# Kernel tuning notes

Measured on AMD Instinct MI355X. Metric: run time of the kernel, lower is better.

## Reference

```python
import jax, jax.numpy as jnp
import numpy as np

B, IN_CH, OUT_CH, R = 16, 32, 32, 32
M1, M2 = 32, 32          # n_modes; must equal in_ch for the torch 2D branch to run
H, W = 256, 256


def setup_inputs() -> dict:
    key = jax.random.key(0)
    k1, k2, k3, k4 = jax.random.split(key, 4)
    x = jax.random.normal(k1, (B, IN_CH, H, W), jnp.float32)
    coeff_real = jax.random.normal(k2, (R, M1, M2, IN_CH), jnp.float32)
    coeff_imag = jax.random.normal(k3, (R, M1, M2, IN_CH), jnp.float32)
    proj = jax.random.normal(k4, (OUT_CH, R), jnp.float32)
    return {"x": x, "coeff_real": coeff_real, "coeff_imag": coeff_imag, "proj": proj}


def reference(x, coeff_real, coeff_imag, proj):
    # rfftn over the last 2 dims -> (B, C, H, W//2+1) complex64
    x_ft = jnp.fft.rfftn(x, axes=(-2, -1))
    coeff = (coeff_real + 1j * coeff_imag).astype(jnp.complex64)  # (R, M1, M2, IN)
    # W = einsum('or, r...i -> o...i') -> axes (OUT, M1, M2, IN)
    Wt = jnp.einsum('or,rabi->oabi', proj.astype(jnp.complex64), coeff)
    Hf, Wf = x_ft.shape[-2], x_ft.shape[-1]
    m1 = min(M1, Hf)   # torch loop bound over i
    m2 = min(M2, Wf)   # torch loop bound over j
    # Faithful to torch indexing: w_slice = W[..., i, j] has shape (OUT, M1) and is
    # contracted against the CHANNEL axis of x_ft. So effectively:
    #   out_ft[b,o,i,j] = sum_c x_ft[b,c,i,j] * Wt[o, c, i, j]
    # where Wt's axis1 (the 'm1' axis) is indexed by channel c.
    sub = jnp.einsum('bcij,ocij->boij', x_ft[..., :m1, :m2], Wt[:, :, :m1, :m2])
    out_ft = jnp.zeros((x.shape[0], OUT_CH, Hf, Wf), jnp.complex64)
    out_ft = out_ft.at[..., :m1, :m2].set(sub.astype(jnp.complex64))
    return jnp.fft.irfftn(out_ft, s=(x.shape[-2], x.shape[-1]), axes=(-2, -1))
```

## Files before the change

### kernel.cpp

```cpp
#include <hip/hip_runtime.h>
#include <math.h>


#define THETA (6.283185307179586f / 256.0f)

typedef float f32x4 __attribute__((ext_vector_type(4)));
typedef __bf16 bf16x8 __attribute__((ext_vector_type(8)));

__device__ __forceinline__ ushort f2bf(float f) {
    uint b = __float_as_uint(f);
    b += 0x7FFF + ((b >> 16) & 1);
    return (ushort)(b >> 16);
}
__device__ __forceinline__ ushort bfc(float f) {
    __bf16 h = (__bf16)f;
    return __builtin_bit_cast(ushort, h);
}

__global__ void kSetup(const float* __restrict__ proj, const float* __restrict__ cr,
                       const float* __restrict__ ci, ushort* __restrict__ Dbf,
                       ushort* __restrict__ Gbf, ushort* __restrict__ Ebf,
                       float2* __restrict__ Wt) {
    int blk = blockIdx.x, tid = threadIdx.x;
    if (blk < 64) {
        float s, c;
        int jr = blk, w = tid;
        __sincosf((((jr >> 1) * w) & 255) * THETA, &s, &c);
        Dbf[jr * 256 + w] = (jr & 1) ? f2bf(-s) : f2bf(c);
        Gbf[w * 64 + jr]  = (jr & 1) ? f2bf(s)  : f2bf(c);
        return;
    }
    if (blk < 128) {
        float s, c;
        int e = (blk - 64) * 256 + tid;
        int h = e >> 6, ir = e & 63;
        __sincosf((((ir >> 1) * h) & 255) * THETA, &s, &c);
        Ebf[h * 64 + ir] = (ir & 1) ? f2bf(-s) : f2bf(c);
        return;
    }
    __shared__ float2 co[32][33];
    __shared__ float pr[32 * 32];
    int bb = blk - 128;
    int c = bb >> 5;
    int i = bb & 31;
    for (int idx = tid; idx < 1024; idx += 256) pr[idx] = proj[idx];
    for (int idx = tid; idx < 1024; idx += 256) {
        int r = idx >> 5, j = idx & 31;
        int g = ((r * 32 + c) * 32 + i) * 32 + j;
        co[r][j] = make_float2(cr[g], ci[g]);
    }
    __syncthreads();
    int j = tid & 31, og = tid >> 5;
    for (int oo = 0; oo < 4; ++oo) {
        int o = og * 4 + oo;
        float wr = 0.f, wi = 0.f;
        #pragma unroll
        for (int r = 0; r < 32; ++r) {
            float p = pr[o * 32 + r];
            float2 v = co[r][j];
            wr += p * v.x;
            wi += p * v.y;
        }
        Wt[((o * 32 + c) * 32 + i) * 32 + j] = make_float2(wr, wi);
    }
}

__global__ void __launch_bounds__(512) kA(const float* __restrict__ x,
                                          const ushort* __restrict__ Dbf,
                                          float2* __restrict__ Xf) {
    __shared__ __align__(16) ushort Dl[64 * 264];
    __shared__ __align__(16) ushort Yl[64 * 264];
    int bc = blockIdx.x;
    int tid = threadIdx.x;
    int l = tid & 63, wv = tid >> 6;
    int lr = l & 15, kg = l >> 4;

    {
        const uint4* ds = (const uint4*)Dbf;
        #pragma unroll
        for (int q = 0; q < 4; ++q) {
            int idx = tid + 512 * q;
            int row = idx >> 5, c8 = idx & 31;
            *(uint4*)&Dl[row * 264 + c8 * 8] = ds[idx];
        }
    }
    __syncthreads();

    const float* xp = x + (size_t)bc * 65536;

    #pragma unroll
    for (int hh = 0; hh < 2; ++hh) {
        f32x4 acc1[4];
        #pragma unroll
        for (int mt = 0; mt < 4; ++mt) acc1[mt] = (f32x4){0.f, 0.f, 0.f, 0.f};
        const f32x4* rp = (const f32x4*)(xp + (size_t)(hh * 128 + wv * 16 + lr) * 256)
                          + kg * 2;
        #pragma unroll
        for (int wh = 0; wh < 2; ++wh) {
            f32x4 xv[8];
            #pragma unroll
            for (int ks = 0; ks < 4; ++ks) {
                xv[2 * ks]     = rp[wh * 32 + ks * 8];
                xv[2 * ks + 1] = rp[wh * 32 + ks * 8 + 1];
            }
            #pragma unroll
            for (int ks = 0; ks < 4; ++ks) {
                bf16x8 b;
                #pragma unroll
                for (int e = 0; e < 4; ++e) {
                    b[e]     = (__bf16)xv[2 * ks][e];
                    b[4 + e] = (__bf16)xv[2 * ks + 1][e];
                }
                bf16x8 a[4];
                #pragma unroll
                for (int mt = 0; mt < 4; ++mt)
                    a[mt] = *(const bf16x8*)&Dl[(mt * 16 + lr) * 264 + wh * 128 + ks * 32 + kg * 8];
                #pragma unroll
                for (int mt = 0; mt < 4; ++mt)
                    acc1[mt] = __builtin_amdgcn_mfma_f32_16x16x32_bf16(
                        a[mt], b, acc1[mt], 0, 0, 0);
            }
        }
        #pragma unroll
        for (int mt = 0; mt < 4; ++mt)
            #pragma unroll
            for (int r = 0; r < 4; ++r) {
                int jr = mt * 16 + kg * 4 + r;
                int row = ((jr & 1) << 5) | (jr >> 1);
                int h = hh * 128 + wv * 16 + lr;
                Yl[row * 264 + h] = bfc(acc1[mt][r]);
            }
    }
    __syncthreads();
    int mh = (wv >> 2) * 2;
    int nc4 = (wv & 3) * 16;
    f32x4 acc2[2];
    #pragma unroll
    for (int m2 = 0; m2 < 2; ++m2) acc2[m2] = (f32x4){0.f, 0.f, 0.f, 0.f};
    #pragma unroll
    for (int ks = 0; ks < 8; ++ks) {
        bf16x8 a[2], b;
        #pragma unroll
        for (int m2 = 0; m2 < 2; ++m2)
            a[m2] = *(const bf16x8*)&Dl[((mh + m2) * 16 + lr) * 264 + ks * 32 + kg * 8];
        b = *(const bf16x8*)&Yl[(nc4 + lr) * 264 + ks * 32 + kg * 8];
        #pragma unroll
        for (int m2 = 0; m2 < 2; ++m2)
            acc2[m2] = __builtin_amdgcn_mfma_f32_16x16x32_bf16(a[m2], b, acc2[m2], 0, 0, 0);
    }
    __syncthreads();
    float* Ol = (float*)Dl;
    #pragma unroll
    for (int m2 = 0; m2 < 2; ++m2)
        #pragma unroll
        for (int r = 0; r < 4; ++r)
            Ol[((mh + m2) * 16 + kg * 4 + r) * 68 + nc4 + lr] = acc2[m2][r];
    __syncthreads();
    #pragma unroll
    for (int q = 0; q < 2; ++q) {
        int idx = tid + 512 * q;
        int i = idx >> 5, j = idx & 31;
        float Xr = Ol[(2 * i) * 68 + j] - Ol[(2 * i + 1) * 68 + 32 + j];
        float Xi = Ol[(2 * i) * 68 + 32 + j] + Ol[(2 * i + 1) * 68 + j];
        Xf[(size_t)bc * 1024 + i * 32 + j] = make_float2(Xr, Xi);
    }
}

__global__ void __launch_bounds__(512) kB(const float2* __restrict__ Xf,
                                          const float2* __restrict__ Wt,
                                          const ushort* __restrict__ Gbf,
                                          const ushort* __restrict__ Ebf,
                                          float* __restrict__ out) {
    __shared__ __align__(16) ushort Al[64 * 72];
    __shared__ __align__(16) ushort Tl[256 * 72];
    int bo = blockIdx.x;
    int b = bo >> 5, o = bo & 31;
    int tid = threadIdx.x;
    int l = tid & 63, wv = tid >> 6;
    int lr = l & 15, kg = l >> 4;
    #pragma unroll
    for (int q = 0; q < 2; ++q) {
        int idx = tid + 512 * q;
        int i = idx >> 5, j = idx & 31;
        const float2* xr = Xf + (size_t)b * 32768 + idx;
        const float2* wr = Wt + (size_t)o * 32768 + idx;
        float orr = 0.f, oi = 0.f;
        #pragma unroll
        for (int c = 0; c < 32; ++c) {
            float2 xv = xr[c * 1024];
            float2 wv = wr[c * 1024];
            orr += xv.x * wv.x - xv.y * wv.y;
            oi  += xv.x * wv.y + xv.y * wv.x;
        }
        float sc = (j ? 2.0f : 1.0f) * (1.0f / 65536.0f);
        Al[(2 * i) * 72 + 2 * j]         = bfc(sc * orr);
        Al[(2 * i) * 72 + 2 * j + 1]     = bfc(-sc * oi);
        Al[(2 * i + 1) * 72 + 2 * j]     = bfc(sc * oi);
        Al[(2 * i + 1) * 72 + 2 * j + 1] = bfc(sc * orr);
    }
    __syncthreads();
    {
        f32x4 acc[4][2];
        #pragma unroll
        for (int mt = 0; mt < 4; ++mt)
            #pragma unroll
            for (int nt = 0; nt < 2; ++nt)
                acc[mt][nt] = (f32x4){0.f, 0.f, 0.f, 0.f};
        #pragma unroll
        for (int ks = 0; ks < 2; ++ks) {
            bf16x8 a[4], b2[2];
            #pragma unroll
            for (int mt = 0; mt < 4; ++mt)
                a[mt] = *(const bf16x8*)&Al[(mt * 16 + lr) * 72 + ks * 32 + kg * 8];
            #pragma unroll
            for (int nt = 0; nt < 2; ++nt)
                b2[nt] = *(const bf16x8*)&Gbf[(wv * 32 + nt * 16 + lr) * 64 + ks * 32 + kg * 8];
            #pragma unroll
            for (int mt = 0; mt < 4; ++mt)
                #pragma unroll
                for (int nt = 0; nt < 2; ++nt)
                    acc[mt][nt] = __builtin_amdgcn_mfma_f32_16x16x32_bf16(
                        a[mt], b2[nt], acc[mt][nt], 0, 0, 0);
        }
        #pragma unroll
        for (int mt = 0; mt < 4; ++mt) {
            int kr0 = mt * 16 + kg * 4;
            #pragma unroll
            for (int nt = 0; nt < 2; ++nt) {
                int w = wv * 32 + nt * 16 + lr;
                ushort4 u = make_ushort4(bfc(acc[mt][nt][0]), bfc(acc[mt][nt][1]),
                                         bfc(acc[mt][nt][2]), bfc(acc[mt][nt][3]));
                *(ushort4*)&Tl[w * 72 + kr0] = u;
            }
        }
    }
    __syncthreads();
    float* op = out + (size_t)bo * 65536;
    for (int nc = 0; nc < 4; ++nc) {
        f32x4 acc[4][2];
        #pragma unroll
        for (int wt = 0; wt < 4; ++wt)
            #pragma unroll
            for (int ht = 0; ht < 2; ++ht)
                acc[wt][ht] = (f32x4){0.f, 0.f, 0.f, 0.f};
        #pragma unroll
        for (int ks = 0; ks < 2; ++ks) {
            bf16x8 aw[4], bh[2];
            #pragma unroll
            for (int wt = 0; wt < 4; ++wt)
                aw[wt] = *(const bf16x8*)&Tl[(nc * 64 + wt * 16 + lr) * 72 + ks * 32 + kg * 8];
            #pragma unroll
            for (int ht = 0; ht < 2; ++ht)
                bh[ht] = *(const bf16x8*)&Ebf[((wv * 2 + ht) * 16 + lr) * 64 + ks * 32 + kg * 8];
            #pragma unroll
            for (int wt = 0; wt < 4; ++wt)
                #pragma unroll
                for (int ht = 0; ht < 2; ++ht)
                    acc[wt][ht] = __builtin_amdgcn_mfma_f32_16x16x32_bf16(
                        aw[wt], bh[ht], acc[wt][ht], 0, 0, 0);
        }
        #pragma unroll
        for (int wt = 0; wt < 4; ++wt)
            #pragma unroll
            for (int ht = 0; ht < 2; ++ht) {
                int h = (wv * 2 + ht) * 16 + lr;
                int w0 = nc * 64 + wt * 16 + kg * 4;
                *(f32x4*)&op[h * 256 + w0] = acc[wt][ht];
            }
    }
}

extern "C" void kernel_launch(void* const* d_in, const int* in_sizes, int n_in,
                              void* d_out, int out_size, void* d_ws, size_t ws_size,
                              hipStream_t stream) {
    const float* x    = (const float*)d_in[0];
    const float* cr   = (const float*)d_in[1];
    const float* ci   = (const float*)d_in[2];
    const float* proj = (const float*)d_in[3];
    float* out = (float*)d_out;
    char* ws = (char*)d_ws;

    float2* Xf  = (float2*)ws;
    float2* Wt  = (float2*)(ws + 4194304);
    ushort* Dbf = (ushort*)(ws + 12582912);
    ushort* Gbf = (ushort*)(ws + 12582912 + 32768);
    ushort* Ebf = (ushort*)(ws + 12582912 + 65536);

    kSetup<<<1152, 256, 0, stream>>>(proj, cr, ci, Dbf, Gbf, Ebf, Wt);
    kA<<<512, 512, 0, stream>>>(x, Dbf, Xf);
    kB<<<512, 512, 0, stream>>>(Xf, Wt, Gbf, Ebf, out);
}
```

Baseline: 84.10 us.

## Split forward DFT kernel into two stages with global bf16 intermediate

The fused forward-transform kernel kA is split into k1, which does the W-axis DFT and writes a bf16 intermediate to global workspace, and k2, which loads that intermediate and does the H-axis DFT to produce the spectrum. The DFT matrix is now read directly from global memory (through the cache) instead of being staged in shared memory. This lowers shared-memory use per block and adds a launch-bounds hint to raise occupancy in the memory-bound first pass. The cost is an extra kernel launch plus a 16 MB intermediate written and read back through global memory.

```diff
diff --git a/kernel.cpp b/kernel.cpp
--- a/kernel.cpp
+++ b/kernel.cpp
@@ -65,27 +65,15 @@
     }
 }
 
-__global__ void __launch_bounds__(512) kA(const float* __restrict__ x,
-                                          const ushort* __restrict__ Dbf,
-                                          float2* __restrict__ Xf) {
-    __shared__ __align__(16) ushort Dl[64 * 264];
+__global__ void __launch_bounds__(512, 4) k1(const float* __restrict__ x,
+                                             const ushort* __restrict__ Dbf,
+                                             ushort* __restrict__ Y1) {
     __shared__ __align__(16) ushort Yl[64 * 264];
     int bc = blockIdx.x;
     int tid = threadIdx.x;
     int l = tid & 63, wv = tid >> 6;
     int lr = l & 15, kg = l >> 4;
 
-    {
-        const uint4* ds = (const uint4*)Dbf;
-        #pragma unroll
-        for (int q = 0; q < 4; ++q) {
-            int idx = tid + 512 * q;
-            int row = idx >> 5, c8 = idx & 31;
-            *(uint4*)&Dl[row * 264 + c8 * 8] = ds[idx];
-        }
-    }
-    __syncthreads();
-
     const float* xp = x + (size_t)bc * 65536;
 
     #pragma unroll
@@ -114,7 +102,7 @@
                 bf16x8 a[4];
                 #pragma unroll
                 for (int mt = 0; mt < 4; ++mt)
-                    a[mt] = *(const bf16x8*)&Dl[(mt * 16 + lr) * 264 + wh * 128 + ks * 32 + kg * 8];
+                    a[mt] = *(const bf16x8*)&Dbf[(mt * 16 + lr) * 256 + wh * 128 + ks * 32 + kg * 8];
                 #pragma unroll
                 for (int mt = 0; mt < 4; ++mt)
                     acc1[mt] = __builtin_amdgcn_mfma_f32_16x16x32_bf16(
@@ -132,33 +120,58 @@
             }
     }
     __syncthreads();
-    int mh = (wv >> 2) * 2;
-    int nc4 = (wv & 3) * 16;
-    f32x4 acc2[2];
-    #pragma unroll
-    for (int m2 = 0; m2 < 2; ++m2) acc2[m2] = (f32x4){0.f, 0.f, 0.f, 0.f};
+    ushort* dst = Y1 + (size_t)bc * 16384;
+    #pragma unroll
+    for (int q = 0; q < 4; ++q) {
+        int idx = tid + 512 * q;
+        int row = idx >> 5, c8 = idx & 31;
+        *(uint4*)&dst[row * 256 + c8 * 8] = *(const uint4*)&Yl[row * 264 + c8 * 8];
+    }
+}
+
+__global__ void __launch_bounds__(256) k2(const ushort* __restrict__ Y1,
+                                          const ushort* __restrict__ Dbf,
+                                          float2* __restrict__ Xf) {
+    __shared__ __align__(16) ushort Bl[64 * 264];
+    int bc = blockIdx.x;
+    int tid = threadIdx.x;
+    int l = tid & 63, wvq = tid >> 6;
+    int lr = l & 15, kg = l >> 4;
+
+    const uint4* src = (const uint4*)(Y1 + (size_t)bc * 16384);
+    #pragma unroll
+    for (int q = 0; q < 8; ++q) {
+        int idx = tid + 256 * q;
+        int row = idx >> 5, c8 = idx & 31;
+        *(uint4*)&Bl[row * 264 + c8 * 8] = src[idx];
+    }
+    __syncthreads();
+    int nc4 = wvq * 16;
+    f32x4 acc2[4];
+    #pragma unroll
+    for (int mt = 0; mt < 4; ++mt) acc2[mt] = (f32x4){0.f, 0.f, 0.f, 0.f};
     #pragma unroll
     for (int ks = 0; ks < 8; ++ks) {
-        bf16x8 a[2], b;
-        #pragma unroll
-        for (int m2 = 0; m2 < 2; ++m2)
-            a[m2] = *(const bf16x8*)&Dl[((mh + m2) * 16 + lr) * 264 + ks * 32 + kg * 8];
-        b = *(const bf16x8*)&Yl[(nc4 + lr) * 264 + ks * 32 + kg * 8];
-        #pragma unroll
-        for (int m2 = 0; m2 < 2; ++m2)
-            acc2[m2] = __builtin_amdgcn_mfma_f32_16x16x32_bf16(a[m2], b, acc2[m2], 0, 0, 0);
-    }
-    __syncthreads();
-    float* Ol = (float*)Dl;
-    #pragma unroll
-    for (int m2 = 0; m2 < 2; ++m2)
+        bf16x8 a[4], b;
+        #pragma unroll
+        for (int mt = 0; mt < 4; ++mt)
+            a[mt] = *(const bf16x8*)&Dbf[(mt * 16 + lr) * 256 + ks * 32 + kg * 8];
+        b = *(const bf16x8*)&Bl[(nc4 + lr) * 264 + ks * 32 + kg * 8];
+        #pragma unroll
+        for (int mt = 0; mt < 4; ++mt)
+            acc2[mt] = __builtin_amdgcn_mfma_f32_16x16x32_bf16(a[mt], b, acc2[mt], 0, 0, 0);
+    }
+    __syncthreads();
+    float* Ol = (float*)Bl;
+    #pragma unroll
+    for (int mt = 0; mt < 4; ++mt)
         #pragma unroll
         for (int r = 0; r < 4; ++r)
-            Ol[((mh + m2) * 16 + kg * 4 + r) * 68 + nc4 + lr] = acc2[m2][r];
-    __syncthreads();
-    #pragma unroll
-    for (int q = 0; q < 2; ++q) {
-        int idx = tid + 512 * q;
+            Ol[(mt * 16 + kg * 4 + r) * 68 + nc4 + lr] = acc2[mt][r];
+    __syncthreads();
+    #pragma unroll
+    for (int q = 0; q < 4; ++q) {
+        int idx = tid + 256 * q;
         int i = idx >> 5, j = idx & 31;
         float Xr = Ol[(2 * i) * 68 + j] - Ol[(2 * i + 1) * 68 + 32 + j];
         float Xi = Ol[(2 * i) * 68 + 32 + j] + Ol[(2 * i + 1) * 68 + j];
@@ -282,11 +295,13 @@
 
     float2* Xf  = (float2*)ws;
     float2* Wt  = (float2*)(ws + 4194304);
-    ushort* Dbf = (ushort*)(ws + 12582912);
-    ushort* Gbf = (ushort*)(ws + 12582912 + 32768);
-    ushort* Ebf = (ushort*)(ws + 12582912 + 65536);
+    ushort* Y1  = (ushort*)(ws + 12582912);
+    ushort* Dbf = (ushort*)(ws + 29360128);
+    ushort* Gbf = (ushort*)(ws + 29360128 + 32768);
+    ushort* Ebf = (ushort*)(ws + 29360128 + 65536);
 
     kSetup<<<1152, 256, 0, stream>>>(proj, cr, ci, Dbf, Gbf, Ebf, Wt);
-    kA<<<512, 512, 0, stream>>>(x, Dbf, Xf);
+    k1<<<512, 512, 0, stream>>>(x, Dbf, Y1);
+    k2<<<512, 256, 0, stream>>>(Y1, Dbf, Xf);
     kB<<<512, 512, 0, stream>>>(Xf, Wt, Gbf, Ebf, out);
 }
```

Measured after the change: 123.1 us. 1.46x slower.

## Split forward DFT across two blocks per image half, sum partials in kB

Applied to the files above, without the earlier changes.

kA now runs two 256-thread blocks per (batch, channel), each handling one half of the H rows. Each block computes a partial H-direction DFT and writes it to a separate Xf buffer, and kB adds the two partials before the channel contraction. This doubles the block count for more parallelism and smaller per-block shared memory, which may raise occupancy. In exchange the Xf workspace doubles, kB reads twice the Xf data, and the D matrix is loaded by twice as many blocks.

```diff
diff --git a/kernel.cpp b/kernel.cpp
--- a/kernel.cpp
+++ b/kernel.cpp
@@ -65,12 +65,13 @@
     }
 }
 
-__global__ void __launch_bounds__(512) kA(const float* __restrict__ x,
+__global__ void __launch_bounds__(256) kA(const float* __restrict__ x,
                                           const ushort* __restrict__ Dbf,
                                           float2* __restrict__ Xf) {
     __shared__ __align__(16) ushort Dl[64 * 264];
-    __shared__ __align__(16) ushort Yl[64 * 264];
-    int bc = blockIdx.x;
+    __shared__ __align__(16) ushort Yl[64 * 136];
+    int blk = blockIdx.x;
+    int hh = blk & 1, bc = blk >> 1;
     int tid = threadIdx.x;
     int l = tid & 63, wv = tid >> 6;
     int lr = l & 15, kg = l >> 4;
@@ -78,10 +79,9 @@
     {
         const uint4* ds = (const uint4*)Dbf;
         #pragma unroll
-        for (int q = 0; q < 4; ++q) {
-            int idx = tid + 512 * q;
-            int row = idx >> 5, c8 = idx & 31;
-            *(uint4*)&Dl[row * 264 + c8 * 8] = ds[idx];
+        for (int q = 0; q < 8; ++q) {
+            int idx = tid + 256 * q;
+            *(uint4*)&Dl[(idx >> 5) * 264 + (idx & 31) * 8] = ds[idx];
         }
     }
     __syncthreads();
@@ -89,12 +89,12 @@
     const float* xp = x + (size_t)bc * 65536;
 
     #pragma unroll
-    for (int hh = 0; hh < 2; ++hh) {
+    for (int ht = 0; ht < 2; ++ht) {
         f32x4 acc1[4];
         #pragma unroll
         for (int mt = 0; mt < 4; ++mt) acc1[mt] = (f32x4){0.f, 0.f, 0.f, 0.f};
-        const f32x4* rp = (const f32x4*)(xp + (size_t)(hh * 128 + wv * 16 + lr) * 256)
-                          + kg * 2;
+        const f32x4* rp = (const f32x4*)(xp +
+            (size_t)(hh * 128 + wv * 32 + ht * 16 + lr) * 256) + kg * 2;
         #pragma unroll
         for (int wh = 0; wh < 2; ++wh) {
             f32x4 xv[8];
@@ -127,42 +127,40 @@
             for (int r = 0; r < 4; ++r) {
                 int jr = mt * 16 + kg * 4 + r;
                 int row = ((jr & 1) << 5) | (jr >> 1);
-                int h = hh * 128 + wv * 16 + lr;
-                Yl[row * 264 + h] = bfc(acc1[mt][r]);
-            }
-    }
-    __syncthreads();
-    int mh = (wv >> 2) * 2;
-    int nc4 = (wv & 3) * 16;
-    f32x4 acc2[2];
-    #pragma unroll
-    for (int m2 = 0; m2 < 2; ++m2) acc2[m2] = (f32x4){0.f, 0.f, 0.f, 0.f};
-    #pragma unroll
-    for (int ks = 0; ks < 8; ++ks) {
-        bf16x8 a[2], b;
-        #pragma unroll
-        for (int m2 = 0; m2 < 2; ++m2)
-            a[m2] = *(const bf16x8*)&Dl[((mh + m2) * 16 + lr) * 264 + ks * 32 + kg * 8];
-        b = *(const bf16x8*)&Yl[(nc4 + lr) * 264 + ks * 32 + kg * 8];
-        #pragma unroll
-        for (int m2 = 0; m2 < 2; ++m2)
-            acc2[m2] = __builtin_amdgcn_mfma_f32_16x16x32_bf16(a[m2], b, acc2[m2], 0, 0, 0);
-    }
-    __syncthreads();
-    float* Ol = (float*)Dl;
-    #pragma unroll
-    for (int m2 = 0; m2 < 2; ++m2)
+                int hcol = wv * 32 + ht * 16 + lr;
+                Yl[row * 136 + hcol] = bfc(acc1[mt][r]);
+            }
+    }
+    __syncthreads();
+    f32x4 acc2[4];
+    #pragma unroll
+    for (int mt = 0; mt < 4; ++mt) acc2[mt] = (f32x4){0.f, 0.f, 0.f, 0.f};
+    #pragma unroll
+    for (int ks = 0; ks < 4; ++ks) {
+        bf16x8 a[4], b;
+        #pragma unroll
+        for (int mt = 0; mt < 4; ++mt)
+            a[mt] = *(const bf16x8*)&Dl[(mt * 16 + lr) * 264 + hh * 128 + ks * 32 + kg * 8];
+        b = *(const bf16x8*)&Yl[(wv * 16 + lr) * 136 + ks * 32 + kg * 8];
+        #pragma unroll
+        for (int mt = 0; mt < 4; ++mt)
+            acc2[mt] = __builtin_amdgcn_mfma_f32_16x16x32_bf16(a[mt], b, acc2[mt], 0, 0, 0);
+    }
+    __syncthreads();
+    float* Ol = (float*)Yl;
+    #pragma unroll
+    for (int mt = 0; mt < 4; ++mt)
         #pragma unroll
         for (int r = 0; r < 4; ++r)
-            Ol[((mh + m2) * 16 + kg * 4 + r) * 68 + nc4 + lr] = acc2[m2][r];
-    __syncthreads();
-    #pragma unroll
-    for (int q = 0; q < 2; ++q) {
-        int idx = tid + 512 * q;
+            Ol[(mt * 16 + kg * 4 + r) * 68 + wv * 16 + lr] = acc2[mt][r];
+    __syncthreads();
+    #pragma unroll
+    for (int q = 0; q < 4; ++q) {
+        int idx = tid + 256 * q;
         int i = idx >> 5, j = idx & 31;
         float Xr = Ol[(2 * i) * 68 + j] - Ol[(2 * i + 1) * 68 + 32 + j];
         float Xi = Ol[(2 * i) * 68 + 32 + j] + Ol[(2 * i + 1) * 68 + j];
-        Xf[(size_t)bc * 1024 + i * 32 + j] = make_float2(Xr, Xi);
+        Xf[(size_t)hh * 524288 + (size_t)bc * 1024 + idx] = make_float2(Xr, Xi);
     }
 }
 
@@ -182,15 +180,18 @@
     for (int q = 0; q < 2; ++q) {
         int idx = tid + 512 * q;
         int i = idx >> 5, j = idx & 31;
-        const float2* xr = Xf + (size_t)b * 32768 + idx;
+        const float2* xr0 = Xf + (size_t)b * 32768 + idx;
+        const float2* xr1 = Xf + 524288 + (size_t)b * 32768 + idx;
         const float2* wr = Wt + (size_t)o * 32768 + idx;
         float orr = 0.f, oi = 0.f;
         #pragma unroll
         for (int c = 0; c < 32; ++c) {
-            float2 xv = xr[c * 1024];
-            float2 wv = wr[c * 1024];
-            orr += xv.x * wv.x - xv.y * wv.y;
-            oi  += xv.x * wv.y + xv.y * wv.x;
+            float2 x0 = xr0[c * 1024];
+            float2 x1 = xr1[c * 1024];
+            float2 wvv = wr[c * 1024];
+            float xvx = x0.x + x1.x, xvy = x0.y + x1.y;
+            orr += xvx * wvv.x - xvy * wvv.y;
+            oi  += xvx * wvv.y + xvy * wvv.x;
         }
         float sc = (j ? 2.0f : 1.0f) * (1.0f / 65536.0f);
         Al[(2 * i) * 72 + 2 * j]         = bfc(sc * orr);
@@ -281,12 +282,12 @@
     char* ws = (char*)d_ws;
 
     float2* Xf  = (float2*)ws;
-    float2* Wt  = (float2*)(ws + 4194304);
-    ushort* Dbf = (ushort*)(ws + 12582912);
-    ushort* Gbf = (ushort*)(ws + 12582912 + 32768);
-    ushort* Ebf = (ushort*)(ws + 12582912 + 65536);
+    float2* Wt  = (float2*)(ws + 8388608);
+    ushort* Dbf = (ushort*)(ws + 16777216);
+    ushort* Gbf = (ushort*)(ws + 16777216 + 32768);
+    ushort* Ebf = (ushort*)(ws + 16777216 + 65536);
 
     kSetup<<<1152, 256, 0, stream>>>(proj, cr, ci, Dbf, Gbf, Ebf, Wt);
-    kA<<<512, 512, 0, stream>>>(x, Dbf, Xf);
+    kA<<<1024, 256, 0, stream>>>(x, Dbf, Xf);
     kB<<<512, 512, 0, stream>>>(Xf, Wt, Gbf, Ebf, out);
 }
```

Result: slower. 101.2 us (+20.3%).
